# Kernel optimization log

Hardware: AMD Instinct MI355X
Metric: run time of the kernel (lower is better)

## Reference

```python
import jax, jax.numpy as jnp
import numpy as np

FEAT = 256
HID = FEAT // 2
N_KEYS = 2          # output_keys = ["energy_0", "energy_1"]
N_MOLS = 2000
ATOMS_PER_MOL = 100
N_ATOMS = N_MOLS * ATOMS_PER_MOL
LOG2 = 0.6931471805599453


def shifted_softplus(x):
    # NFF's shifted softplus: softplus(x) - log(2)
    return jax.nn.softplus(x) - LOG2


def setup_inputs() -> dict:
    key = jax.random.key(0)
    ks = jax.random.split(key, 6)
    s_i = jax.random.normal(ks[0], (N_ATOMS, FEAT), dtype=jnp.float32)
    xyz = jax.random.normal(ks[1], (N_ATOMS, 3), dtype=jnp.float32)
    num_atoms = jnp.full((N_MOLS,), ATOMS_PER_MOL, dtype=jnp.int64)
    # Per-key MLP params stacked over keys: Linear(F->H), act, Linear(H->1)
    W1 = jax.random.normal(ks[2], (N_KEYS, FEAT, HID), dtype=jnp.float32) / np.sqrt(FEAT)
    b1 = jnp.zeros((N_KEYS, HID), dtype=jnp.float32)
    W2 = jax.random.normal(ks[3], (N_KEYS, HID), dtype=jnp.float32) / np.sqrt(HID)
    b2 = jnp.zeros((N_KEYS,), dtype=jnp.float32)
    return {"s_i": s_i, "xyz": xyz, "num_atoms": num_atoms,
            "W1": W1, "b1": b1, "W2": W2, "b2": b2}


def reference(s_i, xyz, num_atoms, W1, b1, W2, b2):
    n_mols = num_atoms.shape[0]
    # segment id per atom, replacing the torch.split(...)+per-chunk sum loop
    seg = jnp.repeat(jnp.arange(n_mols), num_atoms,
                     total_repeat_length=s_i.shape[0])        # [N]
    # per-key MLP: [K,N,H] hidden, [K,N] scalar output per atom
    h = shifted_softplus(jnp.einsum('nf,kfh->knh', s_i, W1) + b1[:, None, :])
    val = jnp.einsum('knh,kh->kn', h, W2) + b2[:, None]       # [K, N]
    # fused segment-sum pooling -> per-molecule scalars
    pooled = jax.ops.segment_sum(val.T, seg, num_segments=n_mols)  # [M, K]
    return pooled.T                                            # [K, M]
```

## Files before the change

### kernel.cpp

```cpp
#include <hip/hip_runtime.h>

#define FEAT 256
#define HID 128
#define NKEYS 2

typedef __bf16 bf16x8 __attribute__((ext_vector_type(8)));
typedef float f32x16 __attribute__((ext_vector_type(16)));

#define LDS_ROW 1040

union Frag {
    bf16x8 v;
    unsigned u[4];
    uint4 q;
};

__device__ __forceinline__ unsigned pack_bf16_u2(unsigned u0, unsigned u1) {
    u0 += 0x8000u;
    u1 += 0x8000u;
    return __builtin_amdgcn_perm(u1, u0, 0x07060302u);
}

__device__ __forceinline__ float ssp(float x) {
    float sp = __logf(1.0f + __expf(x));
    sp = (x > 15.0f) ? x : sp;
    return sp - 0.69314718056f;
}

__device__ __forceinline__ int find_mol(const int* __restrict__ off, int n_mols, int g) {
    int lo = 0, hi = n_mols;
    while (hi - lo > 1) {
        int mid = (lo + hi) >> 1;
        if (off[mid] <= g) lo = mid; else hi = mid;
    }
    return lo;
}

__global__ void prep_kernel(const void* __restrict__ num_atoms_raw,
                            const float* __restrict__ W1,
                            int n_mols, int n_atoms,
                            int* __restrict__ off,
                            unsigned short* __restrict__ Bp2,
                            float* __restrict__ out, int out_n) {
    if (blockIdx.x > 0) {
        int idx = (blockIdx.x - 1) * 256 + threadIdx.x;
        int arr  = (idx >> 15) & 1;
        int w    = (idx >> 13) & 3;
        int c    = (idx >> 11) & 3;
        int jj   = (idx >> 9)  & 3;
        int lane = (idx >> 3)  & 63;
        int e    = idx & 7;
        int l31 = lane & 31, half = lane >> 5;
        int row = w * 64 + l31 + arr * 32;
        int k   = c * 64 + jj * 16 + half * 8 + e;
        int key = row >> 7, jh = row & 127;
        float f = W1[(size_t)key * FEAT * HID + (size_t)k * HID + jh];
        unsigned u = __float_as_uint(f);
        unsigned r = (u + 0x7FFFu + ((u >> 16) & 1u)) >> 16;
        size_t out_idx = ((size_t)(arr * 4096 + ((w * 4 + c) * 4 + jj) * 64 + lane)) * 8 + e;
        Bp2[out_idx] = (unsigned short)r;
        return;
    }
    for (int i = threadIdx.x; i < out_n; i += 256) out[i] = 0.0f;

    __shared__ long long tsum[256];
    __shared__ int csum[257];
    __shared__ int mode_sh;
    int tid = threadIdx.x;
    const int* a32 = (const int*)num_atoms_raw;
    const long long* a64 = (const long long*)num_atoms_raw;
    int chunk = (n_mols + 255) >> 8;
    int lo = tid * chunk;
    if (lo > n_mols) lo = n_mols;
    int hi = lo + chunk;
    if (hi > n_mols) hi = n_mols;
    long long s = 0;
    for (int i = lo; i < hi; ++i) s += (long long)a32[i];
    tsum[tid] = s;
    __syncthreads();
    if (tid == 0) {
        long long t = 0;
        for (int i = 0; i < 256; ++i) t += tsum[i];
        mode_sh = (t == (long long)n_atoms) ? 0 : 1;
    }
    __syncthreads();
    int mode = mode_sh;
    if (mode) {
        s = 0;
        for (int i = lo; i < hi; ++i) s += a64[i];
        tsum[tid] = s;
    }
    csum[tid] = (int)tsum[tid];
    __syncthreads();
    if (tid == 0) {
        int run = 0;
        for (int i = 0; i < 256; ++i) { int v = csum[i]; csum[i] = run; run += v; }
    }
    __syncthreads();
    int run = csum[tid];
    for (int i = lo; i < hi; ++i) {
        off[i] = run;
        run += mode ? (int)a64[i] : a32[i];
    }
    if (hi >= n_mols) off[n_mols] = run;
}

__global__ __launch_bounds__(256, 2)
void gemm_fused(const float* __restrict__ A,
                const uint4* __restrict__ Bp2,
                const float* __restrict__ b1,
                const float* __restrict__ W2,
                const float* __restrict__ b2,
                const int* __restrict__ off,
                float* __restrict__ out,
                int n_atoms, int n_mols) {
    __shared__ unsigned char ldsAraw[64 * LDS_ROW];
    __shared__ float part[4][64];
    __shared__ float molacc[NKEYS][4];

    const int tid  = threadIdx.x;
    const int lane = tid & 63;
    const int wn   = tid >> 6;
    const int l31  = lane & 31;
    const int half = lane >> 5;
    const int m0   = blockIdx.x * 64;

    {
        uint4 q[16];
        #pragma unroll
        for (int i = 0; i < 16; ++i) {
            const int r = wn * 16 + i;
            int grow = m0 + r;
            if (grow > n_atoms - 1) grow = n_atoms - 1;
            q[i] = *(const uint4*)(A + (size_t)grow * FEAT + lane * 4);
        }
        #pragma unroll
        for (int i = 0; i < 16; ++i) {
            const int r = wn * 16 + i;
            *(uint4*)(ldsAraw + r * LDS_ROW + lane * 16) = q[i];
        }
    }

    const uint4* B0 = Bp2;
    const uint4* B1 = Bp2 + 4096;
    Frag bf0[2][4], bf1[2][4];
    #pragma unroll
    for (int s = 0; s < 2; ++s)
        #pragma unroll
        for (int j = 0; j < 4; ++j) {
            bf0[s][j].q = B0[(((wn * 4) + s) * 4 + j) * 64 + lane];
            bf1[s][j].q = B1[(((wn * 4) + s) * 4 + j) * 64 + lane];
        }

    __syncthreads();

    const unsigned char* rbp0 = ldsAraw + l31 * LDS_ROW;
    const unsigned char* rbp1 = ldsAraw + (l31 + 32) * LDS_ROW;

    f32x16 acc00 = 0.0f, acc01 = 0.0f, acc10 = 0.0f, acc11 = 0.0f;

    #pragma unroll
    for (int c = 0; c < 4; ++c) {
        const int slot = c & 1;
        #pragma unroll
        for (int j = 0; j < 4; ++j) {
            const int g0 = (c * 16 + j * 4 + half * 2) * 16;
            uint4 q0 = *(const uint4*)(rbp0 + g0);
            uint4 q1 = *(const uint4*)(rbp0 + g0 + 16);
            uint4 r0 = *(const uint4*)(rbp1 + g0);
            uint4 r1 = *(const uint4*)(rbp1 + g0 + 16);
            Frag a0, a1;
            a0.u[0] = pack_bf16_u2(q0.x, q0.y);
            a0.u[1] = pack_bf16_u2(q0.z, q0.w);
            a0.u[2] = pack_bf16_u2(q1.x, q1.y);
            a0.u[3] = pack_bf16_u2(q1.z, q1.w);
            a1.u[0] = pack_bf16_u2(r0.x, r0.y);
            a1.u[1] = pack_bf16_u2(r0.z, r0.w);
            a1.u[2] = pack_bf16_u2(r1.x, r1.y);
            a1.u[3] = pack_bf16_u2(r1.z, r1.w);
            acc00 = __builtin_amdgcn_mfma_f32_32x32x16_bf16(a0.v, bf0[slot][j].v, acc00, 0, 0, 0);
            acc01 = __builtin_amdgcn_mfma_f32_32x32x16_bf16(a0.v, bf1[slot][j].v, acc01, 0, 0, 0);
            acc10 = __builtin_amdgcn_mfma_f32_32x32x16_bf16(a1.v, bf0[slot][j].v, acc10, 0, 0, 0);
            acc11 = __builtin_amdgcn_mfma_f32_32x32x16_bf16(a1.v, bf1[slot][j].v, acc11, 0, 0, 0);
        }
        if (c + 2 < 4) {
            #pragma unroll
            for (int j = 0; j < 4; ++j) {
                bf0[slot][j].q = B0[(((wn * 4) + (c + 2)) * 4 + j) * 64 + lane];
                bf1[slot][j].q = B1[(((wn * 4) + (c + 2)) * 4 + j) * 64 + lane];
            }
        }
    }

    if (tid < NKEYS * 4) molacc[tid >> 2][tid & 3] = 0.0f;

    const int c0 = wn * 64 + l31;
    float b1c0 = b1[c0], b1c1 = b1[c0 + 32];
    float w2c0 = W2[c0], w2c1 = W2[c0 + 32];

    #pragma unroll
    for (int rt = 0; rt < 2; ++rt) {
        const f32x16& Ac0 = rt ? acc10 : acc00;
        const f32x16& Ac1 = rt ? acc11 : acc01;
        #pragma unroll
        for (int r = 0; r < 16; ++r) {
            float t = ssp(Ac0[r] + b1c0) * w2c0 + ssp(Ac1[r] + b1c1) * w2c1;
            t += __shfl_xor(t, 1);
            t += __shfl_xor(t, 2);
            t += __shfl_xor(t, 4);
            t += __shfl_xor(t, 8);
            t += __shfl_xor(t, 16);
            if (l31 == r) {
                int row = rt * 32 + (r & 3) + 8 * (r >> 2) + 4 * half;
                part[wn][row] = t;
            }
        }
    }
    __syncthreads();

    if (tid < NKEYS * 64) {
        int key = tid >> 6, r = tid & 63;
        int gm = m0 + r;
        if (gm < n_atoms) {
            float val = part[2 * key][r] + part[2 * key + 1][r] + b2[key];
            int mol  = find_mol(off, n_mols, gm);
            int mol0 = find_mol(off, n_mols, m0);
            int ml = mol - mol0;
            if (ml < 4) atomicAdd(&molacc[key][ml], val);
            else        atomicAdd(&out[(size_t)key * n_mols + mol], val);
        }
    }
    __syncthreads();

    if (tid < NKEYS * 4) {
        int key = tid >> 2, ml = tid & 3;
        int mol0 = find_mol(off, n_mols, m0);
        int mol = mol0 + ml;
        if (mol < n_mols) {
            float v = molacc[key][ml];
            if (v != 0.0f) atomicAdd(&out[(size_t)key * n_mols + mol], v);
        }
    }
}

extern "C" void kernel_launch(void* const* d_in, const int* in_sizes, int n_in,
                              void* d_out, int out_size, void* d_ws, size_t ws_size,
                              hipStream_t stream) {
    const float* s_i      = (const float*)d_in[0];
    const void*  num_atoms = d_in[2];
    const float* W1 = (const float*)d_in[3];
    const float* b1 = (const float*)d_in[4];
    const float* W2 = (const float*)d_in[5];
    const float* b2 = (const float*)d_in[6];
    int n_atoms = in_sizes[0] / FEAT;
    int n_mols  = in_sizes[2];
    float* out = (float*)d_out;

    int* off = (int*)d_ws;
    size_t off_bytes = (((size_t)(n_mols + 1) * 4) + 255) & ~(size_t)255;
    unsigned short* Bp2 = (unsigned short*)((char*)d_ws + off_bytes);

    int pack_blocks = (NKEYS * HID * FEAT) / 256;
    prep_kernel<<<1 + pack_blocks, 256, 0, stream>>>(num_atoms, W1, n_mols, n_atoms,
                                                     off, Bp2, out, out_size);

    int gblocks = (n_atoms + 63) / 64;
    gemm_fused<<<gblocks, 256, 0, stream>>>(s_i, (const uint4*)Bp2, b1, W2, b2, off,
                                            out, n_atoms, n_mols);
}
```

Before: 388.2 us.

## Pre-transpose activations into MFMA fragment layout and run LDS-free GEMM

Adds a transpose kernel that converts fp32 activations into bf16 MFMA-fragment-ordered tiles in workspace. A new GEMM kernel then loads A and B fragments directly from global memory with no LDS staging, using 32-row tiles and higher occupancy. The B packing layout is flattened to match. This removes LDS round-trips and the in-loop conversion from the GEMM, but adds an extra global write and read of the converted activations and an extra launch. The old fused kernel is kept as a fallback when the workspace is too small.

```diff
diff --git a/kernel.cpp b/kernel.cpp
--- a/kernel.cpp
+++ b/kernel.cpp
@@ -3,11 +3,11 @@
 #define FEAT 256
 #define HID 128
 #define NKEYS 2
+#define KSTRIDE 258
+#define LDS_ROW 1040
 
 typedef __bf16 bf16x8 __attribute__((ext_vector_type(8)));
 typedef float f32x16 __attribute__((ext_vector_type(16)));
-
-#define LDS_ROW 1040
 
 union Frag {
     bf16x8 v;
@@ -46,18 +46,17 @@
         int idx = (blockIdx.x - 1) * 256 + threadIdx.x;
         int arr  = (idx >> 15) & 1;
         int w    = (idx >> 13) & 3;
-        int c    = (idx >> 11) & 3;
-        int jj   = (idx >> 9)  & 3;
+        int ks   = (idx >> 9)  & 15;
         int lane = (idx >> 3)  & 63;
         int e    = idx & 7;
         int l31 = lane & 31, half = lane >> 5;
         int row = w * 64 + l31 + arr * 32;
-        int k   = c * 64 + jj * 16 + half * 8 + e;
+        int k   = ks * 16 + half * 8 + e;
         int key = row >> 7, jh = row & 127;
         float f = W1[(size_t)key * FEAT * HID + (size_t)k * HID + jh];
         unsigned u = __float_as_uint(f);
         unsigned r = (u + 0x7FFFu + ((u >> 16) & 1u)) >> 16;
-        size_t out_idx = ((size_t)(arr * 4096 + ((w * 4 + c) * 4 + jj) * 64 + lane)) * 8 + e;
+        size_t out_idx = ((size_t)(arr * 4096 + (w * 16 + ks) * 64 + lane)) * 8 + e;
         Bp2[out_idx] = (unsigned short)r;
         return;
     }
@@ -105,15 +104,134 @@
     if (hi >= n_mols) off[n_mols] = run;
 }
 
+__global__ __launch_bounds__(256, 4)
+void transpose_kernel(const float* __restrict__ A, uint4* __restrict__ At,
+                      int n_atoms) {
+    __shared__ float ldsF[32 * KSTRIDE];
+    const int tid  = threadIdx.x;
+    const int w    = tid >> 6;
+    const int lane = tid & 63;
+    const int rt   = blockIdx.x;
+    const int a0   = rt * 32;
+
+    #pragma unroll
+    for (int i = 0; i < 8; ++i) {
+        int atom = i * 4 + w;
+        int ga = a0 + atom;
+        if (ga > n_atoms - 1) ga = n_atoms - 1;
+        float4 v = *(const float4*)(A + (size_t)ga * FEAT + lane * 4);
+        float* d = &ldsF[atom * KSTRIDE + lane * 4];
+        *(float2*)(d)     = make_float2(v.x, v.y);
+        *(float2*)(d + 2) = make_float2(v.z, v.w);
+    }
+    __syncthreads();
+
+    #pragma unroll
+    for (int e = 0; e < 4; ++e) {
+        int f    = e * 4 + w;
+        int atom = lane & 31;
+        int kb   = f * 16 + (lane >> 5) * 8;
+        const float* s = &ldsF[atom * KSTRIDE + kb];
+        uint4 p;
+        p.x = pack_bf16_u2(__float_as_uint(s[0]), __float_as_uint(s[1]));
+        p.y = pack_bf16_u2(__float_as_uint(s[2]), __float_as_uint(s[3]));
+        p.z = pack_bf16_u2(__float_as_uint(s[4]), __float_as_uint(s[5]));
+        p.w = pack_bf16_u2(__float_as_uint(s[6]), __float_as_uint(s[7]));
+        At[((size_t)rt * 16 + f) * 64 + lane] = p;
+    }
+}
+
+__global__ __launch_bounds__(256, 3)
+void gemm_frag(const uint4* __restrict__ At,
+               const uint4* __restrict__ Bp2,
+               const float* __restrict__ b1,
+               const float* __restrict__ W2,
+               const float* __restrict__ b2,
+               const int* __restrict__ off,
+               float* __restrict__ out,
+               int n_atoms, int n_mols) {
+    __shared__ float part[4][32];
+    __shared__ float molacc[NKEYS][4];
+
+    const int tid  = threadIdx.x;
+    const int lane = tid & 63;
+    const int wn   = tid >> 6;
+    const int l31  = lane & 31;
+    const int half = lane >> 5;
+    const int rt   = blockIdx.x;
+    const int m0   = rt * 32;
+
+    const uint4* Ab = At + (size_t)rt * 16 * 64 + lane;
+    const uint4* B0 = Bp2 + (size_t)(wn * 16) * 64 + lane;
+    const uint4* B1 = Bp2 + 4096 + (size_t)(wn * 16) * 64 + lane;
+
+    f32x16 acc0 = 0.0f, acc1 = 0.0f;
+
+    #pragma unroll
+    for (int ks = 0; ks < 16; ++ks) {
+        Frag a, q0, q1;
+        a.q  = Ab[ks * 64];
+        q0.q = B0[ks * 64];
+        q1.q = B1[ks * 64];
+        acc0 = __builtin_amdgcn_mfma_f32_32x32x16_bf16(a.v, q0.v, acc0, 0, 0, 0);
+        acc1 = __builtin_amdgcn_mfma_f32_32x32x16_bf16(a.v, q1.v, acc1, 0, 0, 0);
+    }
+
+    if (tid < NKEYS * 4) molacc[tid >> 2][tid & 3] = 0.0f;
+
+    const int c0 = wn * 64 + l31;
+    float b1c0 = b1[c0], b1c1 = b1[c0 + 32];
+    float w2c0 = W2[c0], w2c1 = W2[c0 + 32];
+
+    #pragma unroll
+    for (int r = 0; r < 16; ++r) {
+        float t = ssp(acc0[r] + b1c0) * w2c0 + ssp(acc1[r] + b1c1) * w2c1;
+        t += __shfl_xor(t, 1);
+        t += __shfl_xor(t, 2);
+        t += __shfl_xor(t, 4);
+        t += __shfl_xor(t, 8);
+        t += __shfl_xor(t, 16);
+        if (l31 == r) {
+            int row = (r & 3) + 8 * (r >> 2) + 4 * half;
+            part[wn][row] = t;
+        }
+    }
+    __syncthreads();
+
+    if (tid < NKEYS * 32) {
+        int key = tid >> 5, r = tid & 31;
+        int gm = m0 + r;
+        if (gm < n_atoms) {
+            float val = part[2 * key][r] + part[2 * key + 1][r] + b2[key];
+            int mol  = find_mol(off, n_mols, gm);
+            int mol0 = find_mol(off, n_mols, m0);
+            int ml = mol - mol0;
+            if (ml < 4) atomicAdd(&molacc[key][ml], val);
+            else        atomicAdd(&out[(size_t)key * n_mols + mol], val);
+        }
+    }
+    __syncthreads();
+
+    if (tid < NKEYS * 4) {
+        int key = tid >> 2, ml = tid & 3;
+        int mol0 = find_mol(off, n_mols, m0);
+        int mol = mol0 + ml;
+        if (mol < n_mols) {
+            float v = molacc[key][ml];
+            if (v != 0.0f) atomicAdd(&out[(size_t)key * n_mols + mol], v);
+        }
+    }
+}
+
 __global__ __launch_bounds__(256, 2)
-void gemm_fused(const float* __restrict__ A,
-                const uint4* __restrict__ Bp2,
-                const float* __restrict__ b1,
-                const float* __restrict__ W2,
-                const float* __restrict__ b2,
-                const int* __restrict__ off,
-                float* __restrict__ out,
-                int n_atoms, int n_mols) {
+void gemm_fallback(const float* __restrict__ A,
+                   const uint4* __restrict__ Bp2,
+                   const float* __restrict__ b1,
+                   const float* __restrict__ W2,
+                   const float* __restrict__ b2,
+                   const int* __restrict__ off,
+                   float* __restrict__ out,
+                   int n_atoms, int n_mols) {
     __shared__ unsigned char ldsAraw[64 * LDS_ROW];
     __shared__ float part[4][64];
     __shared__ float molacc[NKEYS][4];
@@ -148,8 +266,8 @@
     for (int s = 0; s < 2; ++s)
         #pragma unroll
         for (int j = 0; j < 4; ++j) {
-            bf0[s][j].q = B0[(((wn * 4) + s) * 4 + j) * 64 + lane];
-            bf1[s][j].q = B1[(((wn * 4) + s) * 4 + j) * 64 + lane];
+            bf0[s][j].q = B0[(wn * 16 + s * 4 + j) * 64 + lane];
+            bf1[s][j].q = B1[(wn * 16 + s * 4 + j) * 64 + lane];
         }
 
     __syncthreads();
@@ -186,8 +304,8 @@
         if (c + 2 < 4) {
             #pragma unroll
             for (int j = 0; j < 4; ++j) {
-                bf0[slot][j].q = B0[(((wn * 4) + (c + 2)) * 4 + j) * 64 + lane];
-                bf1[slot][j].q = B1[(((wn * 4) + (c + 2)) * 4 + j) * 64 + lane];
+                bf0[slot][j].q = B0[(wn * 16 + (c + 2) * 4 + j) * 64 + lane];
+                bf1[slot][j].q = B1[(wn * 16 + (c + 2) * 4 + j) * 64 + lane];
             }
         }
     }
@@ -199,9 +317,9 @@
     float w2c0 = W2[c0], w2c1 = W2[c0 + 32];
 
     #pragma unroll
-    for (int rt = 0; rt < 2; ++rt) {
-        const f32x16& Ac0 = rt ? acc10 : acc00;
-        const f32x16& Ac1 = rt ? acc11 : acc01;
+    for (int rt2 = 0; rt2 < 2; ++rt2) {
+        const f32x16& Ac0 = rt2 ? acc10 : acc00;
+        const f32x16& Ac1 = rt2 ? acc11 : acc01;
         #pragma unroll
         for (int r = 0; r < 16; ++r) {
             float t = ssp(Ac0[r] + b1c0) * w2c0 + ssp(Ac1[r] + b1c1) * w2c1;
@@ -211,7 +329,7 @@
             t += __shfl_xor(t, 8);
             t += __shfl_xor(t, 16);
             if (l31 == r) {
-                int row = rt * 32 + (r & 3) + 8 * (r >> 2) + 4 * half;
+                int row = rt2 * 32 + (r & 3) + 8 * (r >> 2) + 4 * half;
                 part[wn][row] = t;
             }
         }
@@ -259,12 +377,23 @@
     int* off = (int*)d_ws;
     size_t off_bytes = (((size_t)(n_mols + 1) * 4) + 255) & ~(size_t)255;
     unsigned short* Bp2 = (unsigned short*)((char*)d_ws + off_bytes);
-
-    int pack_blocks = (NKEYS * HID * FEAT) / 256;
-    prep_kernel<<<1 + pack_blocks, 256, 0, stream>>>(num_atoms, W1, n_mols, n_atoms,
-                                                     off, Bp2, out, out_size);
-
-    int gblocks = (n_atoms + 63) / 64;
-    gemm_fused<<<gblocks, 256, 0, stream>>>(s_i, (const uint4*)Bp2, b1, W2, b2, off,
-                                            out, n_atoms, n_mols);
-}
+    const size_t bp2_bytes = 131072;
+
+    int rtcnt = (n_atoms + 31) / 32;
+    size_t at_bytes = (size_t)rtcnt * 16384;
+    size_t need = off_bytes + bp2_bytes + at_bytes;
+
+    prep_kernel<<<257, 256, 0, stream>>>(num_atoms, W1, n_mols, n_atoms,
+                                         off, Bp2, out, out_size);
+
+    if (ws_size >= need) {
+        uint4* At = (uint4*)((char*)d_ws + off_bytes + bp2_bytes);
+        transpose_kernel<<<rtcnt, 256, 0, stream>>>(s_i, At, n_atoms);
+        gemm_frag<<<rtcnt, 256, 0, stream>>>(At, (const uint4*)Bp2, b1, W2, b2,
+                                             off, out, n_atoms, n_mols);
+    } else {
+        int gblocks = (n_atoms + 63) / 64;
+        gemm_fallback<<<gblocks, 256, 0, stream>>>(s_i, (const uint4*)Bp2, b1, W2,
+                                                   b2, off, out, n_atoms, n_mols);
+    }
+}
```

Result: no change. 383.0 us (-1.3%).
